# Kernel optimization log

Measured on AMD Instinct MI355X. Metric: run time of the kernel, lower is better.

The kernel has to match this reference:

```python
import jax, jax.numpy as jnp
import numpy as np
from jax import lax

N_IMG = 2
LEVEL_HW = [(200, 200), (100, 100), (50, 50), (25, 25), (13, 13)]
STRIDES = [4, 8, 16, 32, 64]
SIZES = [32.0, 64.0, 128.0, 256.0, 512.0]
A = 3
LEVEL_SIZES = [A * h * w for h, w in LEVEL_HW]
R = sum(LEVEL_SIZES)  # 159882
PRE_NMS = 1000   # pre_nms_top_n['testing']
POST_NMS = 1000  # post_nms_top_n['testing']
NMS_THRESH = 0.7
SCORE_THRESH = 0.0
MIN_SIZE = 1e-3
IMG_H = IMG_W = 800.0
BBOX_XFORM_CLIP = float(np.log(1000.0 / 16.0))


def _make_anchors():
    ratios = np.array([0.5, 1.0, 2.0])
    h_r = np.sqrt(ratios)
    w_r = 1.0 / h_r
    out = []
    for (h, w), stride, size in zip(LEVEL_HW, STRIDES, SIZES):
        ws = size * w_r
        hs = size * h_r
        base = np.stack([-ws / 2, -hs / 2, ws / 2, hs / 2], 1)  # [A,4]
        sx = (np.arange(w) + 0.5) * stride
        sy = (np.arange(h) + 0.5) * stride
        yy, xx = np.meshgrid(sy, sx, indexing='ij')
        shifts = np.stack([xx.ravel(), yy.ravel(), xx.ravel(), yy.ravel()], 1)  # [H*W,4]
        out.append((shifts[:, None, :] + base[None, :, :]).reshape(-1, 4))
    return np.concatenate(out, 0).astype(np.float32)  # [R,4]


def setup_inputs() -> dict:
    key = jax.random.key(0)
    k1, k2 = jax.random.split(key)
    objectness = jax.random.normal(k1, (N_IMG, R), jnp.float32)
    deltas = jax.random.normal(k2, (N_IMG, R, 4), jnp.float32) * 0.2
    anchors = jnp.asarray(_make_anchors())
    return {"objectness": objectness, "deltas": deltas, "anchors": anchors}


def _decode(deltas, anchors):
    # BoxCoder.decode with weights (1,1,1,1)
    wa = anchors[:, 2] - anchors[:, 0]
    ha = anchors[:, 3] - anchors[:, 1]
    cxa = anchors[:, 0] + 0.5 * wa
    cya = anchors[:, 1] + 0.5 * ha
    dx, dy, dw, dh = deltas[..., 0], deltas[..., 1], deltas[..., 2], deltas[..., 3]
    dw = jnp.minimum(dw, BBOX_XFORM_CLIP)
    dh = jnp.minimum(dh, BBOX_XFORM_CLIP)
    cx = dx * wa + cxa
    cy = dy * ha + cya
    w = jnp.exp(dw) * wa
    h = jnp.exp(dh) * ha
    return jnp.stack([cx - 0.5 * w, cy - 0.5 * h, cx + 0.5 * w, cy + 0.5 * h], -1)


def _nms_single(boxes, scores, lvl, valid):
    # batched_nms via per-level coordinate offset trick
    offs = lvl.astype(boxes.dtype) * (max(IMG_H, IMG_W) + 1.0)
    ob = boxes + offs[:, None]
    s = jnp.where(valid, scores, -1.0)
    order = jnp.argsort(-s)
    b = ob[order]          # offset boxes, score-descending
    raw = boxes[order]     # original boxes
    v = valid[order]
    ss = s[order]
    area = (b[:, 2] - b[:, 0]) * (b[:, 3] - b[:, 1])
    lt = jnp.maximum(b[:, None, :2], b[None, :, :2])
    rb = jnp.minimum(b[:, None, 2:], b[None, :, 2:])
    wh = jnp.clip(rb - lt, 0.0)
    inter = wh[..., 0] * wh[..., 1]
    iou = inter / (area[:, None] + area[None, :] - inter + 1e-9)  # [K,K]
    K = b.shape[0]

    def body(keep, i):
        suppressed = jnp.any(keep & (iou[:, i] > NMS_THRESH))
        keep = keep.at[i].set(v[i] & ~suppressed)
        return keep, None

    keep, _ = lax.scan(body, jnp.zeros((K,), bool), jnp.arange(K))
    # compact kept boxes (score order preserved) into fixed POST_NMS slots
    pos = jnp.where(keep, jnp.minimum(jnp.cumsum(keep) - 1, POST_NMS), POST_NMS)
    out_b = jnp.zeros((POST_NMS + 1, 4), boxes.dtype).at[pos].set(raw)[:POST_NMS]
    out_s = jnp.full((POST_NMS + 1,), -1.0, boxes.dtype).at[pos].set(ss)[:POST_NMS]
    return out_b, out_s


def _forward(objectness, deltas, anchors):
    proposals = _decode(deltas, anchors)  # [N,R,4]
    # per-level topk (pre_nms_top_n)
    idxs = []
    off = 0
    for n in LEVEL_SIZES:
        k = min(PRE_NMS, n)
        _, ti = lax.top_k(objectness[:, off:off + n], k)
        idxs.append(ti + off)
        off += n
    top_idx = jnp.concatenate(idxs, 1)  # [N,K]
    obj = jnp.take_along_axis(objectness, top_idx, 1)
    boxes = jnp.take_along_axis(proposals, top_idx[..., None], 1)
    levels = jnp.concatenate([jnp.full((n,), i, jnp.int32) for i, n in enumerate(LEVEL_SIZES)])
    lvl = levels[top_idx]
    scores = jax.nn.sigmoid(obj)
    # clip_boxes_to_image
    x1 = jnp.clip(boxes[..., 0], 0.0, IMG_W)
    y1 = jnp.clip(boxes[..., 1], 0.0, IMG_H)
    x2 = jnp.clip(boxes[..., 2], 0.0, IMG_W)
    y2 = jnp.clip(boxes[..., 3], 0.0, IMG_H)
    boxes = jnp.stack([x1, y1, x2, y2], -1)
    # remove_small_boxes + score_thresh -> validity mask (fixed shapes)
    valid = (x2 - x1 >= MIN_SIZE) & (y2 - y1 >= MIN_SIZE) & (scores >= SCORE_THRESH)
    return jax.vmap(_nms_single)(boxes, scores, lvl, valid)


def reference(objectness, deltas, anchors):
    return _forward(objectness, deltas, anchors)
```

## Files before the change

kernel.cpp:

```cpp
#include <hip/hip_runtime.h>

typedef unsigned long long u64;
typedef unsigned int u32;

#define R_TOT 159882
#define POST 1000
#define IMG_SZ 800.0f
#define NMS_TH 0.7f
#define BBOX_CLIP 4.135166556742356f
#define LCAP 1024

__device__ __forceinline__ float fadd_(float a, float b){ return __fadd_rn(a,b); }
__device__ __forceinline__ float fsub_(float a, float b){ return __fsub_rn(a,b); }
__device__ __forceinline__ float fmul_(float a, float b){ return __fmul_rn(a,b); }

__device__ __forceinline__ int lvl_len(int l){ const int L[5]={120000,30000,7500,1875,507}; return L[l]; }
__device__ __forceinline__ int lvl_off(int l){ const int L[5]={0,120000,150000,157500,159375}; return L[l]; }
__device__ __forceinline__ int lvl_k(int l){ const int L[5]={1000,1000,1000,1000,507}; return L[l]; }

__device__ __forceinline__ u32 mono_(u32 u){ return (u & 0x80000000u) ? ~u : (u | 0x80000000u); }

__device__ __forceinline__ u64 readlane64(u64 v, int i){
  u32 lo = (u32)__builtin_amdgcn_readlane((int)(u32)v, i);
  u32 hi = (u32)__builtin_amdgcn_readlane((int)(u32)(v >> 32), i);
  return ((u64)hi << 32) | (u64)lo;
}

__global__ __launch_bounds__(256) void k_hist(const float* __restrict__ obj, int* hist16){
  int g = blockIdx.x, sl = blockIdx.y;
  int img = g/5, lvl = g%5;
  int n = lvl_len(lvl), s0 = lvl_off(lvl);
  __shared__ int lh[4096];
  int tid = threadIdx.x;
  for (int i = tid; i < 4096; i += 256) lh[i] = 0;
  __syncthreads();
  int lo = (int)((long long)n * sl / 16), hiS = (int)((long long)n * (sl+1) / 16);
  const float* p = obj + img*R_TOT + s0;
  #pragma unroll 4
  for (int e = lo + tid; e < hiS; e += 256){
    u32 mu = mono_(__float_as_uint(p[e]));
    atomicAdd(&lh[(~mu) >> 20], 1);
  }
  __syncthreads();
  int* dst = hist16 + (g*16 + sl)*4096;
  for (int i = tid; i < 4096; i += 256) dst[i] = lh[i];
}

__global__ __launch_bounds__(1024) void k_sel(const float* __restrict__ obj,
                                              const float4* __restrict__ deltas,
                                              const float4* __restrict__ anchors,
                                              const int* __restrict__ hist16,
                                              float4* boxL, float* scoreL,
                                              float4* nbox, u64* okeyN, int* ncnt){
  int g = blockIdx.x, img = g/5, lvl = g%5;
  int s0 = lvl_off(lvl), n = lvl_len(lvl), k = lvl_k(lvl);
  const float* p = obj + img*R_TOT + s0;
  __shared__ u64 lmain[1024];
  __shared__ u64 lbuf2[1024];
  __shared__ float4 lbox[1024];
  __shared__ u64 lokey[1024];
  __shared__ unsigned char lval[1024];
  __shared__ int wsum[16];
  __shared__ int h16s[16];
  __shared__ int sh_bs, sh_rem, sh_sc, lc, lc2;
  __shared__ u64 sh_thr;
  int tid = threadIdx.x, lane = tid & 63, wid = tid >> 6;

  if (tid == 0){ lc = 0; lc2 = 0; sh_sc = 0; }
  lmain[tid] = ~0ull;

  int h0 = 0, h1 = 0, h2 = 0, h3 = 0;
  {
    const int* hb = hist16 + g*16*4096 + 4*tid;
    #pragma unroll
    for (int sl = 0; sl < 16; sl++){
      int4 a = *(const int4*)(hb + sl*4096);
      h0 += a.x; h1 += a.y; h2 += a.z; h3 += a.w;
    }
  }
  int part = h0 + h1 + h2 + h3;
  int x = part;
  for (int d = 1; d < 64; d <<= 1){ int y = __shfl_up(x, d); if (lane >= d) x += y; }
  if (lane == 63) wsum[wid] = x;
  __syncthreads();
  int add = 0;
  for (int w = 0; w < wid; w++) add += wsum[w];
  int incl = x + add, excl = incl - part;
  if (excl < k && k <= incl){
    int cum = excl;
    if (cum + h0 >= k){ sh_bs = 4*tid;   sh_rem = k - cum; }
    else { cum += h0;
      if (cum + h1 >= k){ sh_bs = 4*tid+1; sh_rem = k - cum; }
      else { cum += h1;
        if (cum + h2 >= k){ sh_bs = 4*tid+2; sh_rem = k - cum; }
        else { cum += h2;    sh_bs = 4*tid+3; sh_rem = k - cum; }
      }
    }
  }
  __syncthreads();
  int bs = sh_bs, rem0 = sh_rem;

  for (int e0 = tid; e0 < n; e0 += 8192){
    float v[8];
    #pragma unroll
    for (int q = 0; q < 8; q++){
      int e = e0 + q*1024;
      v[q] = (e < n) ? p[e] : 0.0f;
    }
    #pragma unroll
    for (int q = 0; q < 8; q++){
      int e = e0 + q*1024;
      if (e < n){
        u32 mu = mono_(__float_as_uint(v[q]));
        u64 key56 = (((u64)(~mu)) << 24) | (u32)(s0 + e);
        int bin = (int)(key56 >> 44);
        if (bin < bs){ int pos = atomicAdd(&lc, 1); lmain[pos] = key56; }
        else if (bin == bs){ int pos = atomicAdd(&lc2, 1); if (pos < 1024) lbuf2[pos] = key56; }
      }
    }
  }
  __syncthreads();
  int nb = lc, c2 = lc2;

  if (c2 <= LCAP){
    for (int e = tid; e < c2; e += 1024){
      u64 kk = lbuf2[e];
      int rk = 0;
      for (int q = 0; q < c2; q++) rk += (lbuf2[q] < kk) ? 1 : 0;
      if (rk < rem0){ int p2 = atomicAdd(&sh_sc, 1); lmain[nb + p2] = kk; }
    }
  } else {
    if (tid == 0) sh_thr = ((u64)bs) << 44;
    __syncthreads();
    for (int shift = 40; shift >= 0; shift -= 4){
      if (tid < 16) h16s[tid] = 0;
      __syncthreads();
      u64 pref = sh_thr;
      u64 himask = ~((1ull << (shift+4)) - 1ull);
      for (int e = tid; e < n; e += 1024){
        u32 mu = mono_(__float_as_uint(p[e]));
        u64 kk = (((u64)(~mu)) << 24) | (u32)(s0 + e);
        if ((kk & himask) == (pref & himask)) atomicAdd(&h16s[(int)((kk >> shift) & 15)], 1);
      }
      __syncthreads();
      if (tid == 0){
        int r2 = sh_rem, cum = 0;
        for (int d = 0; d < 16; d++){
          int hb2 = h16s[d];
          if (cum + hb2 >= r2){ sh_thr = pref | ((u64)d << shift); sh_rem = r2 - cum; break; }
          cum += hb2;
        }
      }
      __syncthreads();
    }
    u64 thr = sh_thr;
    for (int e = tid; e < n; e += 1024){
      u32 mu = mono_(__float_as_uint(p[e]));
      u64 kk = (((u64)(~mu)) << 24) | (u32)(s0 + e);
      if ((int)(kk >> 44) == bs && kk <= thr){ int p2 = atomicAdd(&sh_sc, 1); lmain[nb + p2] = kk; }
    }
  }
  __syncthreads();

  for (int k2 = 2; k2 <= 1024; k2 <<= 1){
    for (int j = k2 >> 1; j > 0; j >>= 1){
      __syncthreads();
      int i = tid, ixj = i ^ j;
      if (ixj > i){
        u64 a = lmain[i], b = lmain[ixj];
        bool up = (i & k2) == 0;
        if ((a > b) == up){ lmain[i] = b; lmain[ixj] = a; }
      }
    }
  }
  __syncthreads();

  int r = tid, t = g*1024 + r;
  if (r < k){
    int idx = (int)(lmain[r] & 0xFFFFFFu);
    float4 a = anchors[idx];
    float4 d = deltas[img*R_TOT + idx];
    float o = obj[img*R_TOT + idx];
    float wa = fsub_(a.z, a.x), ha = fsub_(a.w, a.y);
    float cxa = fadd_(a.x, fmul_(0.5f, wa)), cya = fadd_(a.y, fmul_(0.5f, ha));
    float dw = fminf(d.z, BBOX_CLIP), dh = fminf(d.w, BBOX_CLIP);
    float cx = fadd_(fmul_(d.x, wa), cxa), cy = fadd_(fmul_(d.y, ha), cya);
    float w  = fmul_(expf(dw), wa),        h  = fmul_(expf(dh), ha);
    float x1 = fsub_(cx, fmul_(0.5f, w)), y1 = fsub_(cy, fmul_(0.5f, h));
    float x2 = fadd_(cx, fmul_(0.5f, w)), y2 = fadd_(cy, fmul_(0.5f, h));
    x1 = fminf(fmaxf(x1, 0.0f), IMG_SZ); y1 = fminf(fmaxf(y1, 0.0f), IMG_SZ);
    x2 = fminf(fmaxf(x2, 0.0f), IMG_SZ); y2 = fminf(fmaxf(y2, 0.0f), IMG_SZ);
    bool valid = (fsub_(x2, x1) >= 1e-3f) && (fsub_(y2, y1) >= 1e-3f);
    float e = expf(-o);
    float sig = __fdiv_rn(1.0f, fadd_(1.0f, e));
    float s = valid ? sig : -1.0f;
    u32 sb = __float_as_uint(s);
    u32 ms = (sb & 0x80000000u) ? ~sb : (sb | 0x80000000u);
    float4 b4 = make_float4(x1, y1, x2, y2);
    boxL[t] = b4;
    scoreL[t] = sig;
    lokey[r] = (((u64)(~ms)) << 32) | (u32)(lvl*1000 + r);
    lbox[r] = b4;
    lval[r] = valid ? 1 : 0;
  } else {
    lval[r] = 0;
  }
  __syncthreads();

  if (tid < 64){
    int cnt = 0;
    float off = (float)lvl * 801.0f;
    for (int base = 0; base < k; base += 64){
      int r2 = base + lane;
      bool v = (r2 < k) && lval[r2];
      float4 b = lbox[r2 < k ? r2 : 0];
      u64 mask = __ballot(v);
      int before = __popcll(mask & ((1ull << lane) - 1ull));
      if (v){
        int pos = cnt + before;
        nbox[g*1024 + pos] = make_float4(fadd_(b.x,off), fadd_(b.y,off), fadd_(b.z,off), fadd_(b.w,off));
        okeyN[g*1024 + pos] = lokey[r2];
      }
      cnt += __popcll(mask);
    }
    if (lane == 0) ncnt[g] = cnt;
  }
}

__global__ __launch_bounds__(64) void k_mask(const float4* __restrict__ nbox,
                                             const int* __restrict__ ncnt,
                                             u64* LTG2){
  int g = blockIdx.x, tr = blockIdx.y, tw = blockIdx.z;
  if (tw > tr) return;
  int m = ncnt[g];
  if (tr*64 >= m) return;
  __shared__ float4 shb[64];
  int lane = threadIdx.x;
  if (tw*64 + lane < m) shb[lane] = nbox[g*1024 + tw*64 + lane];
  __syncthreads();
  int j = tr*64 + lane;
  if (j >= m) return;
  float4 a = nbox[g*1024 + j];
  float areaA = fmul_(fsub_(a.z,a.x), fsub_(a.w,a.y));
  int imax = m - tw*64; if (imax > 64) imax = 64;
  if (tw == tr){
    u64 bitsF = 0;
    for (int ii = lane+1; ii < imax; ii++){
      float4 b = shb[ii];
      float ltx = fmaxf(a.x, b.x), lty = fmaxf(a.y, b.y);
      float rbx = fminf(a.z, b.z), rby = fminf(a.w, b.w);
      float wx = fmaxf(fsub_(rbx, ltx), 0.0f), wy = fmaxf(fsub_(rby, lty), 0.0f);
      float inter = fmul_(wx, wy);
      float areaB = fmul_(fsub_(b.z,b.x), fsub_(b.w,b.y));
      float den = fadd_(fsub_(fadd_(areaA, areaB), inter), 1e-9f);
      if (__fdiv_rn(inter, den) > NMS_TH) bitsF |= (1ull << ii);
    }
    LTG2[((size_t)(g*1024 + j))*16 + 15] = bitsF;
  } else {
    u64 bits = 0;
    for (int ii = 0; ii < imax; ii++){
      float4 b = shb[ii];
      float ltx = fmaxf(a.x, b.x), lty = fmaxf(a.y, b.y);
      float rbx = fminf(a.z, b.z), rby = fminf(a.w, b.w);
      float wx = fmaxf(fsub_(rbx, ltx), 0.0f), wy = fmaxf(fsub_(rby, lty), 0.0f);
      float inter = fmul_(wx, wy);
      float areaB = fmul_(fsub_(b.z,b.x), fsub_(b.w,b.y));
      float den = fadd_(fsub_(fadd_(areaA, areaB), inter), 1e-9f);
      if (__fdiv_rn(inter, den) > NMS_TH) bits |= (1ull << ii);
    }
    LTG2[((size_t)(g*1024 + j))*16 + tw] = bits;
  }
}

struct ChunkBuf {
  ulonglong2 v0, v1, v2, v3, v4, v5, v6, v7;
  u64 ok;
};

__device__ __forceinline__ void issue_chunk(const u64* __restrict__ LT2,
                                            const u64* __restrict__ oK,
                                            int c, int lane, ChunkBuf& b){
  int row = c*64 + lane;
  const ulonglong2* rp = (const ulonglong2*)(LT2 + (size_t)row*16);
  b.v0 = rp[0]; b.v1 = rp[1]; b.v2 = rp[2]; b.v3 = rp[3];
  b.v4 = rp[4]; b.v5 = rp[5]; b.v6 = rp[6]; b.v7 = rp[7];
  b.ok = oK[row];
}

__device__ __forceinline__ void consume_chunk(const ChunkBuf& b, int c, int m, int lane,
                                              u64* KwR, u64* runsL, int& cnt){
  int row = c*64 + lane;
  bool inr = row < m;
  u64 supp = 0;
  #define TERM(q, val) supp |= (((q) < c) ? (val) : 0ull) & KwR[q];
  TERM(0,  b.v0.x) TERM(1,  b.v0.y) TERM(2,  b.v1.x) TERM(3,  b.v1.y)
  TERM(4,  b.v2.x) TERM(5,  b.v2.y) TERM(6,  b.v3.x) TERM(7,  b.v3.y)
  TERM(8,  b.v4.x) TERM(9,  b.v4.y) TERM(10, b.v5.x) TERM(11, b.v5.y)
  TERM(12, b.v6.x) TERM(13, b.v6.y) TERM(14, b.v7.x)
  #undef TERM
  u64 fwd = inr ? b.v7.y : 0;
  u64 live = __ballot(inr && (supp == 0));
  u64 fz = __ballot(fwd != 0);
  u64 kept = 0;
  while (1){
    u64 lf = live & fz;
    if (!lf){ kept |= live; break; }
    int i = __builtin_ctzll(lf);
    u64 bi = 1ull << i;
    u64 below = live & (bi - 1ull);
    kept |= below | bi;
    live &= ~(below | bi);
    live &= ~readlane64(fwd, i);
  }
  KwR[c] = kept;
  bool kp = (kept >> lane) & 1ull;
  int before = __popcll(kept & ((1ull << lane) - 1ull));
  if (kp) runsL[cnt + before] = b.ok;
  cnt += __popcll(kept);
}

__global__ __launch_bounds__(1024) void k_scanmerge(const u64* __restrict__ LTG2,
                                                    const int* __restrict__ ncnt,
                                                    const u64* __restrict__ okeyN,
                                                    const float4* __restrict__ boxL,
                                                    const float* __restrict__ scoreL,
                                                    float* out){
  int img = blockIdx.x, tid = threadIdx.x, lane = tid & 63, wid = tid >> 6;
  __shared__ u64 runs[5*1024];
  __shared__ u64 Kw[5][16];
  __shared__ int cl[5];
  if (wid < 5){
    int l = wid, g = img*5 + l;
    int m = ncnt[g];
    int nch = (m + 63) >> 6;
    const u64* LT2 = LTG2 + ((size_t)g*1024)*16;
    const u64* oK = okeyN + g*1024;
    u64* KwR = &Kw[l][0];
    u64* runsL = &runs[l*1024];
    int cnt = 0;
    ChunkBuf A, B;
    if (nch > 0){
      issue_chunk(LT2, oK, 0, lane, A);
      int c = 0;
      while (c < nch){
        if (c+1 < nch) issue_chunk(LT2, oK, c+1, lane, B);
        consume_chunk(A, c, m, lane, KwR, runsL, cnt);
        c++;
        if (c >= nch) break;
        if (c+1 < nch) issue_chunk(LT2, oK, c+1, lane, A);
        consume_chunk(B, c, m, lane, KwR, runsL, cnt);
        c++;
      }
    }
    if (lane == 0) cl[l] = cnt;
  } else {
    for (int t = tid - 320; t < POST; t += 704){
      out[img*POST*4 + t*4 + 0] = 0.0f;
      out[img*POST*4 + t*4 + 1] = 0.0f;
      out[img*POST*4 + t*4 + 2] = 0.0f;
      out[img*POST*4 + t*4 + 3] = 0.0f;
      out[2*POST*4 + img*POST + t] = -1.0f;
    }
  }
  __syncthreads();
  for (int idx = tid; idx < 5*1024; idx += 1024){
    int l = idx >> 10, i = idx & 1023;
    if (i < cl[l]){
      u64 key = runs[l*1024 + i];
      int o0 = l+1; if (o0 >= 5) o0 -= 5;
      int o1 = l+2; if (o1 >= 5) o1 -= 5;
      int o2 = l+3; if (o2 >= 5) o2 -= 5;
      int o3 = l+4; if (o3 >= 5) o3 -= 5;
      const u64* r0 = runs + (o0 << 10);
      const u64* r1 = runs + (o1 << 10);
      const u64* r2 = runs + (o2 << 10);
      const u64* r3 = runs + (o3 << 10);
      int lo0 = 0, hi0 = cl[o0];
      int lo1 = 0, hi1 = cl[o1];
      int lo2 = 0, hi2 = cl[o2];
      int lo3 = 0, hi3 = cl[o3];
      #pragma unroll 1
      for (int st = 0; st < 11; st++){
        int m0 = (lo0+hi0)>>1, m1 = (lo1+hi1)>>1, m2 = (lo2+hi2)>>1, m3 = (lo3+hi3)>>1;
        u64 a0 = r0[m0], a1 = r1[m1], a2 = r2[m2], a3 = r3[m3];
        if (lo0 < hi0){ if (a0 < key) lo0 = m0+1; else hi0 = m0; }
        if (lo1 < hi1){ if (a1 < key) lo1 = m1+1; else hi1 = m1; }
        if (lo2 < hi2){ if (a2 < key) lo2 = m2+1; else hi2 = m2; }
        if (lo3 < hi3){ if (a3 < key) lo3 = m3+1; else hi3 = m3; }
      }
      int rank = i + lo0 + lo1 + lo2 + lo3;
      if (rank < POST){
        int pos = (int)(key & 0xFFFFFFFFull);
        int lvl = pos / 1000, r = pos - lvl*1000;
        int gg = img*5 + lvl;
        float4 bo = boxL[gg*1024 + r];
        float sc = scoreL[gg*1024 + r];
        out[img*POST*4 + rank*4 + 0] = bo.x;
        out[img*POST*4 + rank*4 + 1] = bo.y;
        out[img*POST*4 + rank*4 + 2] = bo.z;
        out[img*POST*4 + rank*4 + 3] = bo.w;
        out[2*POST*4 + img*POST + rank] = sc;
      }
    }
  }
}

extern "C" void kernel_launch(void* const* d_in, const int* in_sizes, int n_in,
                              void* d_out, int out_size, void* d_ws, size_t ws_size,
                              hipStream_t stream){
  (void)in_sizes; (void)n_in; (void)out_size; (void)ws_size;
  const float*  obj     = (const float*)d_in[0];
  const float4* deltas  = (const float4*)d_in[1];
  const float4* anchors = (const float4*)d_in[2];
  float* out = (float*)d_out;
  char* ws = (char*)d_ws;
  int* hist16  = (int*)(ws + 0);
  float4* boxL = (float4*)(ws + 2621440);
  float* scoreL= (float*)(ws + 2785280);
  u64* okeyN   = (u64*)(ws + 2826240);
  float4* nbox = (float4*)(ws + 2908160);
  u64* LTG2    = (u64*)(ws + 3072000);
  int* ncnt    = (int*)(ws + 4382720);

  {
    dim3 gh(10, 16);
    k_hist<<<gh, 256, 0, stream>>>(obj, hist16);
  }
  k_sel<<<10, 1024, 0, stream>>>(obj, deltas, anchors, hist16, boxL, scoreL, nbox, okeyN, ncnt);
  {
    dim3 gm(10, 16, 16);
    k_mask<<<gm, 64, 0, stream>>>(nbox, ncnt, LTG2);
  }
  k_scanmerge<<<2, 1024, 0, stream>>>(LTG2, ncnt, okeyN, boxL, scoreL, out);
}
```

Measured before the change: 169.7 us.

## Fuse NMS IoU mask computation into selection kernel using shared-memory boxes

Removes the separate k_mask launch and computes the pairwise IoU suppression bitmask inside k_sel, reading compacted boxes from a new shared-memory array instead of a global nbox buffer. This saves one kernel launch and a global round-trip for the boxes. In exchange, the mask work (136 tile pairs per group) now runs on only 10 blocks of 16 waves instead of 2560 small blocks, so parallelism drops sharply. The candidate scan loop is also split into a bounds-check-free main part and a guarded tail.

```diff
diff --git a/kernel.cpp b/kernel.cpp
--- a/kernel.cpp
+++ b/kernel.cpp
@@ -51,18 +51,19 @@
                                               const float4* __restrict__ anchors,
                                               const int* __restrict__ hist16,
                                               float4* boxL, float* scoreL,
-                                              float4* nbox, u64* okeyN, int* ncnt){
+                                              u64* okeyN, int* ncnt, u64* LTG2){
   int g = blockIdx.x, img = g/5, lvl = g%5;
   int s0 = lvl_off(lvl), n = lvl_len(lvl), k = lvl_k(lvl);
   const float* p = obj + img*R_TOT + s0;
   __shared__ u64 lmain[1024];
   __shared__ u64 lbuf2[1024];
   __shared__ float4 lbox[1024];
+  __shared__ float4 cbox[1024];
   __shared__ u64 lokey[1024];
   __shared__ unsigned char lval[1024];
   __shared__ int wsum[16];
   __shared__ int h16s[16];
-  __shared__ int sh_bs, sh_rem, sh_sc, lc, lc2;
+  __shared__ int sh_bs, sh_rem, sh_sc, lc, lc2, sh_m;
   __shared__ u64 sh_thr;
   int tid = threadIdx.x, lane = tid & 63, wid = tid >> 6;
 
@@ -100,16 +101,33 @@
   __syncthreads();
   int bs = sh_bs, rem0 = sh_rem;
 
-  for (int e0 = tid; e0 < n; e0 += 8192){
+  {
+    int full = n >> 13;
+    for (int it = 0; it < full; it++){
+      int e0 = (it << 13) + tid;
+      float v[8];
+      #pragma unroll
+      for (int q = 0; q < 8; q++) v[q] = p[e0 + (q << 10)];
+      #pragma unroll
+      for (int q = 0; q < 8; q++){
+        int e = e0 + (q << 10);
+        u32 mu = mono_(__float_as_uint(v[q]));
+        u64 key56 = (((u64)(~mu)) << 24) | (u32)(s0 + e);
+        int bin = (int)(key56 >> 44);
+        if (bin < bs){ int pos = atomicAdd(&lc, 1); lmain[pos] = key56; }
+        else if (bin == bs){ int pos = atomicAdd(&lc2, 1); if (pos < 1024) lbuf2[pos] = key56; }
+      }
+    }
+    int e0 = (full << 13) + tid;
     float v[8];
     #pragma unroll
     for (int q = 0; q < 8; q++){
-      int e = e0 + q*1024;
+      int e = e0 + (q << 10);
       v[q] = (e < n) ? p[e] : 0.0f;
     }
     #pragma unroll
     for (int q = 0; q < 8; q++){
-      int e = e0 + q*1024;
+      int e = e0 + (q << 10);
       if (e < n){
         u32 mu = mono_(__float_as_uint(v[q]));
         u64 key56 = (((u64)(~mu)) << 24) | (u32)(s0 + e);
@@ -218,57 +236,55 @@
       int before = __popcll(mask & ((1ull << lane) - 1ull));
       if (v){
         int pos = cnt + before;
-        nbox[g*1024 + pos] = make_float4(fadd_(b.x,off), fadd_(b.y,off), fadd_(b.z,off), fadd_(b.w,off));
+        cbox[pos] = make_float4(fadd_(b.x,off), fadd_(b.y,off), fadd_(b.z,off), fadd_(b.w,off));
         okeyN[g*1024 + pos] = lokey[r2];
       }
       cnt += __popcll(mask);
     }
-    if (lane == 0) ncnt[g] = cnt;
-  }
-}
-
-__global__ __launch_bounds__(64) void k_mask(const float4* __restrict__ nbox,
-                                             const int* __restrict__ ncnt,
-                                             u64* LTG2){
-  int g = blockIdx.x, tr = blockIdx.y, tw = blockIdx.z;
-  if (tw > tr) return;
-  int m = ncnt[g];
-  if (tr*64 >= m) return;
-  __shared__ float4 shb[64];
-  int lane = threadIdx.x;
-  if (tw*64 + lane < m) shb[lane] = nbox[g*1024 + tw*64 + lane];
-  __syncthreads();
-  int j = tr*64 + lane;
-  if (j >= m) return;
-  float4 a = nbox[g*1024 + j];
-  float areaA = fmul_(fsub_(a.z,a.x), fsub_(a.w,a.y));
-  int imax = m - tw*64; if (imax > 64) imax = 64;
-  if (tw == tr){
-    u64 bitsF = 0;
-    for (int ii = lane+1; ii < imax; ii++){
-      float4 b = shb[ii];
-      float ltx = fmaxf(a.x, b.x), lty = fmaxf(a.y, b.y);
-      float rbx = fminf(a.z, b.z), rby = fminf(a.w, b.w);
-      float wx = fmaxf(fsub_(rbx, ltx), 0.0f), wy = fmaxf(fsub_(rby, lty), 0.0f);
-      float inter = fmul_(wx, wy);
-      float areaB = fmul_(fsub_(b.z,b.x), fsub_(b.w,b.y));
-      float den = fadd_(fsub_(fadd_(areaA, areaB), inter), 1e-9f);
-      if (__fdiv_rn(inter, den) > NMS_TH) bitsF |= (1ull << ii);
-    }
-    LTG2[((size_t)(g*1024 + j))*16 + 15] = bitsF;
-  } else {
-    u64 bits = 0;
-    for (int ii = 0; ii < imax; ii++){
-      float4 b = shb[ii];
-      float ltx = fmaxf(a.x, b.x), lty = fmaxf(a.y, b.y);
-      float rbx = fminf(a.z, b.z), rby = fminf(a.w, b.w);
-      float wx = fmaxf(fsub_(rbx, ltx), 0.0f), wy = fmaxf(fsub_(rby, lty), 0.0f);
-      float inter = fmul_(wx, wy);
-      float areaB = fmul_(fsub_(b.z,b.x), fsub_(b.w,b.y));
-      float den = fadd_(fsub_(fadd_(areaA, areaB), inter), 1e-9f);
-      if (__fdiv_rn(inter, den) > NMS_TH) bits |= (1ull << ii);
-    }
-    LTG2[((size_t)(g*1024 + j))*16 + tw] = bits;
+    if (lane == 0){ ncnt[g] = cnt; sh_m = cnt; }
+  }
+  __syncthreads();
+
+  {
+    int m = sh_m;
+    for (int item = wid; item < 136; item += 16){
+      int tr = 0;
+      while ((tr+1)*(tr+2)/2 <= item) tr++;
+      int tw = item - tr*(tr+1)/2;
+      if (tr*64 >= m) continue;
+      int j = tr*64 + lane;
+      if (j >= m) continue;
+      float4 a = cbox[j];
+      float areaA = fmul_(fsub_(a.z,a.x), fsub_(a.w,a.y));
+      int imax = m - tw*64; if (imax > 64) imax = 64;
+      if (tw == tr){
+        u64 bitsF = 0;
+        for (int ii = lane+1; ii < imax; ii++){
+          float4 b = cbox[tw*64 + ii];
+          float ltx = fmaxf(a.x, b.x), lty = fmaxf(a.y, b.y);
+          float rbx = fminf(a.z, b.z), rby = fminf(a.w, b.w);
+          float wx = fmaxf(fsub_(rbx, ltx), 0.0f), wy = fmaxf(fsub_(rby, lty), 0.0f);
+          float inter = fmul_(wx, wy);
+          float areaB = fmul_(fsub_(b.z,b.x), fsub_(b.w,b.y));
+          float den = fadd_(fsub_(fadd_(areaA, areaB), inter), 1e-9f);
+          if (__fdiv_rn(inter, den) > NMS_TH) bitsF |= (1ull << ii);
+        }
+        LTG2[((size_t)(g*1024 + j))*16 + 15] = bitsF;
+      } else {
+        u64 bits = 0;
+        for (int ii = 0; ii < imax; ii++){
+          float4 b = cbox[tw*64 + ii];
+          float ltx = fmaxf(a.x, b.x), lty = fmaxf(a.y, b.y);
+          float rbx = fminf(a.z, b.z), rby = fminf(a.w, b.w);
+          float wx = fmaxf(fsub_(rbx, ltx), 0.0f), wy = fmaxf(fsub_(rby, lty), 0.0f);
+          float inter = fmul_(wx, wy);
+          float areaB = fmul_(fsub_(b.z,b.x), fsub_(b.w,b.y));
+          float den = fadd_(fsub_(fadd_(areaA, areaB), inter), 1e-9f);
+          if (__fdiv_rn(inter, den) > NMS_TH) bits |= (1ull << ii);
+        }
+        LTG2[((size_t)(g*1024 + j))*16 + tw] = bits;
+      }
+    }
   }
 }
 
@@ -418,18 +434,16 @@
   float4* boxL = (float4*)(ws + 2621440);
   float* scoreL= (float*)(ws + 2785280);
   u64* okeyN   = (u64*)(ws + 2826240);
-  float4* nbox = (float4*)(ws + 2908160);
-  u64* LTG2    = (u64*)(ws + 3072000);
-  int* ncnt    = (int*)(ws + 4382720);
+  u64* LTG2    = (u64*)(ws + 2908160);
+  int* ncnt    = (int*)(ws + 4218880);
 
   {
     dim3 gh(10, 16);
     k_hist<<<gh, 256, 0, stream>>>(obj, hist16);
   }
-  k_sel<<<10, 1024, 0, stream>>>(obj, deltas, anchors, hist16, boxL, scoreL, nbox, okeyN, ncnt);
+  k_sel<<<10, 1024, 0, stream>>>(obj, deltas, anchors, hist16, boxL, scoreL, okeyN, ncnt, LTG2);
   {
-    dim3 gm(10, 16, 16);
-    k_mask<<<gm, 64, 0, stream>>>(nbox, ncnt, LTG2);
-  }
-  k_scanmerge<<<2, 1024, 0, stream>>>(LTG2, ncnt, okeyN, boxL, scoreL, out);
-}
+    dim3 gm(2);
+    k_scanmerge<<<gm, 1024, 0, stream>>>(LTG2, ncnt, okeyN, boxL, scoreL, out);
+  }
+}
```

New measurement: 275.1 us. +62.1%, slower.
